# Kernel tuning notes

Measured on AMD Instinct MI355X. Metric: run time of the kernel, lower is better.

## Reference

```python
import jax, jax.numpy as jnp
import numpy as np


def setup_inputs() -> dict:
    key = jax.random.key(0)
    ks = jax.random.split(key, 5)
    B, C, T, Hh, Ww = 4, 64, 8, 32, 32
    HID = 32
    s = 0.05  # weight scale for numerically sane softmax logits
    return {
        "H": jax.random.normal(ks[0], (B, C, T, Hh, Ww), dtype=jnp.float32),
        "h": jax.random.normal(ks[1], (B, C, Hh, Ww), dtype=jnp.float32),
        "w_q": jax.random.normal(ks[2], (HID, C), dtype=jnp.float32) * s,
        "w_kv": jax.random.normal(ks[3], (HID, C), dtype=jnp.float32) * s,
        "w_o": jax.random.normal(ks[4], (C, HID), dtype=jnp.float32) * s,
    }


def reference(H, h, w_q, w_kv, w_o):
    B, C, T, Hh, Ww = H.shape
    N = Hh * Ww
    Hf = H.reshape(B, C, T, N)
    # 1x1 convs are pure channel-mixing matmuls
    H_kv = jnp.einsum('dc,bctn->bdtn', w_kv, Hf)                # [B, hid, T, N]
    h_q = jnp.einsum('dc,bchw->bdhw', w_q, h).reshape(B, -1, N)  # [B, hid, N]
    h_q = h_q.transpose(0, 2, 1)                                 # [B, N, hid]
    # per-timestep scores, vectorized over t: [B, T, N, N]
    a = jnp.einsum('bnd,bdtm->btnm', h_q, H_kv)
    # remove the diagonal of each per-timestep [N, N] block
    diag = jnp.einsum('btnn->btn', a)                            # [B, T, N]
    eye = jnp.eye(N, dtype=a.dtype)
    a = a - diag[..., :, None] * eye
    # concat over t along rows, softmax over the (T*N) row axis
    att = jax.nn.softmax(a.reshape(B, T * N, N), axis=1)         # [B, T*N, N]
    h_v = jnp.einsum('bdk,bkm->bdm', H_kv.reshape(B, -1, T * N), att)  # [B, hid, N]
    h_v = jnp.einsum('cd,bdhw->bchw', w_o, h_v.reshape(B, -1, Hh, Ww))
    return (h + h_v, att)
```

## Files before the change

### kernel.cpp

```cpp
#include <hip/hip_runtime.h>

typedef short bf16x8 __attribute__((ext_vector_type(8)));
typedef float f32x4  __attribute__((ext_vector_type(4)));
typedef unsigned short ushort_t;

#define HID 32
#define CC  64
#define TT  8
#define NN  1024
#define BB  4
#define KTOT 8192

__device__ __forceinline__ ushort_t f2b(float x) {
    unsigned int u = __float_as_uint(x);
    return (ushort_t)((u + 0x7fffu + ((u >> 16) & 1u)) >> 16);
}
__device__ __forceinline__ float b2f(ushort_t u) {
    return __uint_as_float((unsigned int)u << 16);
}

__global__ __launch_bounds__(256) void k_pre(const float* __restrict__ H,
                                             const float* __restrict__ h,
                                             const float* __restrict__ wq,
                                             const float* __restrict__ wkv,
                                             ushort_t* __restrict__ hqHI,
                                             ushort_t* __restrict__ hqLO,
                                             ushort_t* __restrict__ hkTH0,
                                             ushort_t* __restrict__ hkTH1,
                                             ushort_t* __restrict__ hkTL0,
                                             ushort_t* __restrict__ hkTL1,
                                             ushort_t* __restrict__ hkDB) {
    int bx = blockIdx.x;
    if (bx < 256) {
        int gid = bx * 256 + threadIdx.x;
        int dg = gid >> 15;
        int rest = gid & 32767;
        int b = rest >> 13, tn = rest & 8191;
        int d0 = dg << 4;
        float acc[16];
#pragma unroll
        for (int d = 0; d < 16; d++) acc[d] = 0.f;
        const float* Hb = H + (size_t)(b * CC) * KTOT + tn;
        const float* wb = wkv + d0 * CC;
#pragma unroll 8
        for (int c = 0; c < CC; c++) {
            float v = Hb[(size_t)c * KTOT];
#pragma unroll
            for (int d = 0; d < 16; d++) acc[d] += wb[d * CC + c] * v;
        }
        ushort_t thi[16], tlo[16];
#pragma unroll
        for (int d = 0; d < 16; d++) {
            ushort_t hi = f2b(acc[d]);
            thi[d] = hi;
            tlo[d] = f2b(acc[d] - b2f(hi));
        }
        size_t po = ((size_t)b * KTOT + tn) * 16;
        bf16x8* ohi = (bf16x8*)((dg ? hkTH1 : hkTH0) + po);
        bf16x8* olo = (bf16x8*)((dg ? hkTL1 : hkTL0) + po);
#pragma unroll
        for (int v8 = 0; v8 < 2; v8++) {
            bf16x8 a, l;
#pragma unroll
            for (int j = 0; j < 8; j++) { a[j] = (short)thi[v8*8+j]; l[j] = (short)tlo[v8*8+j]; }
            ohi[v8] = a; olo[v8] = l;
        }
#pragma unroll
        for (int d = 0; d < 16; d++)
            hkDB[((size_t)(b * HID) + d0 + d) * KTOT + tn] = thi[d];
    } else {
        int gid = (bx - 256) * 256 + threadIdx.x;
        int b = gid >> 10;
        float acc[HID];
#pragma unroll
        for (int d = 0; d < HID; d++) acc[d] = 0.f;
        const float* hb = h + (size_t)(b * CC) * NN + (gid & 1023);
#pragma unroll 4
        for (int c = 0; c < CC; c++) {
            float v = hb[c * NN];
#pragma unroll
            for (int d = 0; d < HID; d++) acc[d] += wq[d * CC + c] * v;
        }
        bf16x8* ohi = (bf16x8*)(hqHI + (size_t)gid * HID);
        bf16x8* olo = (bf16x8*)(hqLO + (size_t)gid * HID);
#pragma unroll
        for (int v8 = 0; v8 < 4; v8++) {
            bf16x8 thi, tlo;
#pragma unroll
            for (int j = 0; j < 8; j++) {
                float x = acc[v8 * 8 + j];
                ushort_t hi = f2b(x);
                thi[j] = (short)hi;
                tlo[j] = (short)f2b(x - b2f(hi));
            }
            ohi[v8] = thi; olo[v8] = tlo;
        }
    }
}

__global__ __launch_bounds__(1024) void k_fuse(const ushort_t* __restrict__ hqHI,
                                               const ushort_t* __restrict__ hqLO,
                                               const ushort_t* __restrict__ hkTH0,
                                               const ushort_t* __restrict__ hkTH1,
                                               const ushort_t* __restrict__ hkTL0,
                                               const ushort_t* __restrict__ hkTL1,
                                               const ushort_t* __restrict__ hkDB,
                                               float* __restrict__ att,
                                               float* __restrict__ hv2) {
    int bx = blockIdx.x;
    int b = bx >> 6, mt = bx & 63;
    int mb = mt << 4;
    int tid = threadIdx.x;
    int wave = tid >> 6, lane = tid & 63;
    int g = lane >> 4, c = lane & 15;
    int t = wave >> 1;
    int nh = (wave & 1) << 9;

    __shared__ float csred[16][16];
    __shared__ float hvred[16][16][32];
    __shared__ __align__(16) ushort_t PT[16][16][40];

    size_t ako = ((size_t)b * KTOT + t * NN + (mb + c)) * 16 + (g & 1) * 8;
    bf16x8 akh = *(const bf16x8*)(((g >> 1) ? hkTH1 : hkTH0) + ako);
    bf16x8 akl = *(const bf16x8*)(((g >> 1) ? hkTL1 : hkTL0) + ako);

    const ushort_t* qhi = hqHI + ((size_t)(b << 10)) * HID;
    const ushort_t* qlo = hqLO + ((size_t)(b << 10)) * HID;

    f32x4 cs = {0.f, 0.f, 0.f, 0.f};
    for (int s16 = 0; s16 < 32; s16 += 2) {
        int nbA = nh + s16 * 16, nbB = nbA + 16;
        size_t aoA = (size_t)(nbA + c) * HID + 8 * g;
        size_t aoB = (size_t)(nbB + c) * HID + 8 * g;
        bf16x8 qhA = *(const bf16x8*)(qhi + aoA);
        bf16x8 qlA = *(const bf16x8*)(qlo + aoA);
        bf16x8 qhB = *(const bf16x8*)(qhi + aoB);
        bf16x8 qlB = *(const bf16x8*)(qlo + aoB);
        f32x4 svA = __builtin_amdgcn_mfma_f32_16x16x32_bf16(akh, qlA, (f32x4){0.f,0.f,0.f,0.f}, 0, 0, 0);
        f32x4 svB = __builtin_amdgcn_mfma_f32_16x16x32_bf16(akh, qlB, (f32x4){0.f,0.f,0.f,0.f}, 0, 0, 0);
        svA = __builtin_amdgcn_mfma_f32_16x16x32_bf16(akl, qhA, svA, 0, 0, 0);
        svB = __builtin_amdgcn_mfma_f32_16x16x32_bf16(akl, qhB, svB, 0, 0, 0);
        svA = __builtin_amdgcn_mfma_f32_16x16x32_bf16(akh, qhA, svA, 0, 0, 0);
        svB = __builtin_amdgcn_mfma_f32_16x16x32_bf16(akh, qhB, svB, 0, 0, 0);
        int nA = nbA + c, nB = nbB + c;
#pragma unroll
        for (int r = 0; r < 4; r++) {
            float xA = (nA == mb + 4 * g + r) ? 0.f : svA[r];
            float xB = (nB == mb + 4 * g + r) ? 0.f : svB[r];
            cs[r] += __expf(xA) + __expf(xB);
        }
    }
#pragma unroll
    for (int off = 1; off <= 8; off <<= 1) {
#pragma unroll
        for (int r = 0; r < 4; r++) cs[r] += __shfl_xor(cs[r], off, 64);
    }
    if (c == 0) *(f32x4*)&csred[wave][4 * g] = cs;
    __syncthreads();
    f32x4 gs = {0.f, 0.f, 0.f, 0.f};
#pragma unroll
    for (int w = 0; w < 16; w++)
        gs += *(const f32x4*)&csred[w][4 * g];
    f32x4 vinv;
#pragma unroll
    for (int r = 0; r < 4; r++) vinv[r] = 1.0f / gs[r];

    const ushort_t* vb0 = hkDB + (size_t)(b * HID + c) * KTOT;
    const ushort_t* vb1 = hkDB + (size_t)(b * HID + 16 + c) * KTOT;
    float* attb = att + (size_t)b * KTOT * NN;
    ushort_t (*pt)[40] = PT[wave];

    f32x4 acc0 = {0.f,0.f,0.f,0.f}, acc1 = {0.f,0.f,0.f,0.f};

    for (int ks = 0; ks < 16; ks++) {
        int k0 = t * NN + nh + ks * 32;
#pragma unroll
        for (int half = 0; half < 2; half++) {
            int nb = nh + ks * 32 + half * 16;
            size_t qo = (size_t)(nb + c) * HID + 8 * g;
            bf16x8 qh = *(const bf16x8*)(qhi + qo);
            bf16x8 ql = *(const bf16x8*)(qlo + qo);
            f32x4 sv = __builtin_amdgcn_mfma_f32_16x16x32_bf16(akh, ql, (f32x4){0.f,0.f,0.f,0.f}, 0, 0, 0);
            sv = __builtin_amdgcn_mfma_f32_16x16x32_bf16(akl, qh, sv, 0, 0, 0);
            sv = __builtin_amdgcn_mfma_f32_16x16x32_bf16(akh, qh, sv, 0, 0, 0);
            int n = nb + c;
            float e0, e1, e2, e3;
            {
                float x0 = (n == mb + 4 * g + 0) ? 0.f : sv[0];
                float x1 = (n == mb + 4 * g + 1) ? 0.f : sv[1];
                float x2 = (n == mb + 4 * g + 2) ? 0.f : sv[2];
                float x3 = (n == mb + 4 * g + 3) ? 0.f : sv[3];
                e0 = __expf(x0) * vinv[0];
                e1 = __expf(x1) * vinv[1];
                e2 = __expf(x2) * vinv[2];
                e3 = __expf(x3) * vinv[3];
            }
            f32x4 ev; ev[0] = e0; ev[1] = e1; ev[2] = e2; ev[3] = e3;
            __builtin_nontemporal_store(ev,
                (f32x4*)(attb + (size_t)(t * NN + n) * NN + mb + 4 * g));
            int kl = half * 16 + c;
            pt[4 * g + 0][kl] = f2b(e0);
            pt[4 * g + 1][kl] = f2b(e1);
            pt[4 * g + 2][kl] = f2b(e2);
            pt[4 * g + 3][kl] = f2b(e3);
        }
        bf16x8 pa = *(const bf16x8*)&pt[c][8 * g];
        bf16x8 v0 = *(const bf16x8*)(vb0 + k0 + 8 * g);
        bf16x8 v1 = *(const bf16x8*)(vb1 + k0 + 8 * g);
        acc0 = __builtin_amdgcn_mfma_f32_16x16x32_bf16(pa, v0, acc0, 0, 0, 0);
        acc1 = __builtin_amdgcn_mfma_f32_16x16x32_bf16(pa, v1, acc1, 0, 0, 0);
    }

#pragma unroll
    for (int r = 0; r < 4; r++) {
        hvred[wave][4 * g + r][c]      = acc0[r];
        hvred[wave][4 * g + r][16 + c] = acc1[r];
    }
    __syncthreads();
    if (tid < 512) {
        int m = tid >> 5, d = tid & 31;
        float s = 0.f;
#pragma unroll
        for (int w = 0; w < 16; w++) s += hvred[w][m][d];
        hv2[((size_t)(b << 10) + mb + m) * HID + d] = s;
    }
}

__global__ __launch_bounds__(512) void k_out(const float* __restrict__ h,
                                             const float* __restrict__ wo,
                                             const float* __restrict__ hv2,
                                             float* __restrict__ out0) {
    int bx = blockIdx.x;
    int b = bx >> 6, mt = bx & 63;
    int m0 = mt * 16;
    int tid = threadIdx.x;
    __shared__ float hvL[16][33];
    {
        int mm = tid >> 5, d = tid & 31;
        hvL[mm][d] = hv2[((size_t)(b << 10) + m0 + mm) * HID + d];
    }
    __syncthreads();
#pragma unroll
    for (int i0 = 0; i0 < 2; i0++) {
        int i = i0 * 512 + tid;
        int c = i >> 4, mm = i & 15;
        float v = h[(size_t)(b * CC + c) * NN + m0 + mm];
#pragma unroll
        for (int d = 0; d < HID; d++) v += wo[c * HID + d] * hvL[mm][d];
        out0[(size_t)(b * CC + c) * NN + m0 + mm] = v;
    }
}

extern "C" void kernel_launch(void* const* d_in, const int* in_sizes, int n_in,
                              void* d_out, int out_size, void* d_ws, size_t ws_size,
                              hipStream_t stream) {
    const float* H   = (const float*)d_in[0];
    const float* h   = (const float*)d_in[1];
    const float* wq  = (const float*)d_in[2];
    const float* wkv = (const float*)d_in[3];
    const float* wo  = (const float*)d_in[4];

    float* out0 = (float*)d_out;
    float* att  = out0 + (size_t)BB * CC * NN;

    ushort_t* hqHI  = (ushort_t*)d_ws;
    ushort_t* hqLO  = hqHI  + 131072;
    ushort_t* hkTH0 = hqLO  + 131072;
    ushort_t* hkTH1 = hkTH0 + 524288;
    ushort_t* hkTL0 = hkTH1 + 524288;
    ushort_t* hkTL1 = hkTL0 + 524288;
    ushort_t* hkDB  = hkTL1 + 524288;
    float* hv2  = (float*)(hkDB + 1048576);

    k_pre <<<272, 256,  0, stream>>>(H, h, wq, wkv, hqHI, hqLO,
                                     hkTH0, hkTH1, hkTL0, hkTL1, hkDB);
    k_fuse<<<256, 1024, 0, stream>>>(hqHI, hqLO, hkTH0, hkTH1, hkTL0, hkTL1, hkDB,
                                     att, hv2);
    k_out <<<256, 512,  0, stream>>>(h, wo, hv2, out0);
}
```

Before: 88.50 us.

## Fuse softmax denominator pass with PV accumulation and defer normalization

The separate first pass that only computed column sums of exp is removed. Sums now accumulate inside the P·V loop, which uses a single hi-only bf16 MFMA for the scores, and the 1/sum scaling is applied to the accumulator afterwards. A third loop recomputes the full-precision scores to write the normalized attention output. The block index is also remapped to interleave batches across blocks. The hi-only scores make the denominator and hv slightly less accurate than the stored att values, and the att write no longer overlaps the PV MFMA work.

```diff
diff --git a/kernel.cpp b/kernel.cpp
--- a/kernel.cpp
+++ b/kernel.cpp
@@ -108,7 +108,8 @@
                                                float* __restrict__ att,
                                                float* __restrict__ hv2) {
     int bx = blockIdx.x;
-    int b = bx >> 6, mt = bx & 63;
+    int logical = ((bx & 7) << 5) | (bx >> 3);
+    int b = logical >> 6, mt = logical & 63;
     int mb = mt << 4;
     int tid = threadIdx.x;
     int wave = tid >> 6, lane = tid & 63;
@@ -126,52 +127,12 @@
 
     const ushort_t* qhi = hqHI + ((size_t)(b << 10)) * HID;
     const ushort_t* qlo = hqLO + ((size_t)(b << 10)) * HID;
-
-    f32x4 cs = {0.f, 0.f, 0.f, 0.f};
-    for (int s16 = 0; s16 < 32; s16 += 2) {
-        int nbA = nh + s16 * 16, nbB = nbA + 16;
-        size_t aoA = (size_t)(nbA + c) * HID + 8 * g;
-        size_t aoB = (size_t)(nbB + c) * HID + 8 * g;
-        bf16x8 qhA = *(const bf16x8*)(qhi + aoA);
-        bf16x8 qlA = *(const bf16x8*)(qlo + aoA);
-        bf16x8 qhB = *(const bf16x8*)(qhi + aoB);
-        bf16x8 qlB = *(const bf16x8*)(qlo + aoB);
-        f32x4 svA = __builtin_amdgcn_mfma_f32_16x16x32_bf16(akh, qlA, (f32x4){0.f,0.f,0.f,0.f}, 0, 0, 0);
-        f32x4 svB = __builtin_amdgcn_mfma_f32_16x16x32_bf16(akh, qlB, (f32x4){0.f,0.f,0.f,0.f}, 0, 0, 0);
-        svA = __builtin_amdgcn_mfma_f32_16x16x32_bf16(akl, qhA, svA, 0, 0, 0);
-        svB = __builtin_amdgcn_mfma_f32_16x16x32_bf16(akl, qhB, svB, 0, 0, 0);
-        svA = __builtin_amdgcn_mfma_f32_16x16x32_bf16(akh, qhA, svA, 0, 0, 0);
-        svB = __builtin_amdgcn_mfma_f32_16x16x32_bf16(akh, qhB, svB, 0, 0, 0);
-        int nA = nbA + c, nB = nbB + c;
-#pragma unroll
-        for (int r = 0; r < 4; r++) {
-            float xA = (nA == mb + 4 * g + r) ? 0.f : svA[r];
-            float xB = (nB == mb + 4 * g + r) ? 0.f : svB[r];
-            cs[r] += __expf(xA) + __expf(xB);
-        }
-    }
-#pragma unroll
-    for (int off = 1; off <= 8; off <<= 1) {
-#pragma unroll
-        for (int r = 0; r < 4; r++) cs[r] += __shfl_xor(cs[r], off, 64);
-    }
-    if (c == 0) *(f32x4*)&csred[wave][4 * g] = cs;
-    __syncthreads();
-    f32x4 gs = {0.f, 0.f, 0.f, 0.f};
-#pragma unroll
-    for (int w = 0; w < 16; w++)
-        gs += *(const f32x4*)&csred[w][4 * g];
-    f32x4 vinv;
-#pragma unroll
-    for (int r = 0; r < 4; r++) vinv[r] = 1.0f / gs[r];
-
     const ushort_t* vb0 = hkDB + (size_t)(b * HID + c) * KTOT;
     const ushort_t* vb1 = hkDB + (size_t)(b * HID + 16 + c) * KTOT;
-    float* attb = att + (size_t)b * KTOT * NN;
     ushort_t (*pt)[40] = PT[wave];
 
+    f32x4 cs = {0.f, 0.f, 0.f, 0.f};
     f32x4 acc0 = {0.f,0.f,0.f,0.f}, acc1 = {0.f,0.f,0.f,0.f};
-
     for (int ks = 0; ks < 16; ks++) {
         int k0 = t * NN + nh + ks * 32;
 #pragma unroll
@@ -179,25 +140,13 @@
             int nb = nh + ks * 32 + half * 16;
             size_t qo = (size_t)(nb + c) * HID + 8 * g;
             bf16x8 qh = *(const bf16x8*)(qhi + qo);
-            bf16x8 ql = *(const bf16x8*)(qlo + qo);
-            f32x4 sv = __builtin_amdgcn_mfma_f32_16x16x32_bf16(akh, ql, (f32x4){0.f,0.f,0.f,0.f}, 0, 0, 0);
-            sv = __builtin_amdgcn_mfma_f32_16x16x32_bf16(akl, qh, sv, 0, 0, 0);
-            sv = __builtin_amdgcn_mfma_f32_16x16x32_bf16(akh, qh, sv, 0, 0, 0);
+            f32x4 sv = __builtin_amdgcn_mfma_f32_16x16x32_bf16(akh, qh, (f32x4){0.f,0.f,0.f,0.f}, 0, 0, 0);
             int n = nb + c;
-            float e0, e1, e2, e3;
-            {
-                float x0 = (n == mb + 4 * g + 0) ? 0.f : sv[0];
-                float x1 = (n == mb + 4 * g + 1) ? 0.f : sv[1];
-                float x2 = (n == mb + 4 * g + 2) ? 0.f : sv[2];
-                float x3 = (n == mb + 4 * g + 3) ? 0.f : sv[3];
-                e0 = __expf(x0) * vinv[0];
-                e1 = __expf(x1) * vinv[1];
-                e2 = __expf(x2) * vinv[2];
-                e3 = __expf(x3) * vinv[3];
-            }
-            f32x4 ev; ev[0] = e0; ev[1] = e1; ev[2] = e2; ev[3] = e3;
-            __builtin_nontemporal_store(ev,
-                (f32x4*)(attb + (size_t)(t * NN + n) * NN + mb + 4 * g));
+            float e0 = __expf((n == mb + 4 * g + 0) ? 0.f : sv[0]);
+            float e1 = __expf((n == mb + 4 * g + 1) ? 0.f : sv[1]);
+            float e2 = __expf((n == mb + 4 * g + 2) ? 0.f : sv[2]);
+            float e3 = __expf((n == mb + 4 * g + 3) ? 0.f : sv[3]);
+            cs[0] += e0; cs[1] += e1; cs[2] += e2; cs[3] += e3;
             int kl = half * 16 + c;
             pt[4 * g + 0][kl] = f2b(e0);
             pt[4 * g + 1][kl] = f2b(e1);
@@ -210,12 +159,49 @@
         acc0 = __builtin_amdgcn_mfma_f32_16x16x32_bf16(pa, v0, acc0, 0, 0, 0);
         acc1 = __builtin_amdgcn_mfma_f32_16x16x32_bf16(pa, v1, acc1, 0, 0, 0);
     }
+#pragma unroll
+    for (int off = 1; off <= 8; off <<= 1) {
+        cs[0] += __shfl_xor(cs[0], off, 64);
+        cs[1] += __shfl_xor(cs[1], off, 64);
+        cs[2] += __shfl_xor(cs[2], off, 64);
+        cs[3] += __shfl_xor(cs[3], off, 64);
+    }
+    if (c == 0) *(f32x4*)&csred[wave][4 * g] = cs;
+    __syncthreads();
+    f32x4 gs = {0.f, 0.f, 0.f, 0.f};
+#pragma unroll
+    for (int w = 0; w < 16; w++)
+        gs += *(const f32x4*)&csred[w][4 * g];
+    f32x4 vinv;
+#pragma unroll
+    for (int r = 0; r < 4; r++) vinv[r] = 1.0f / gs[r];
 
 #pragma unroll
     for (int r = 0; r < 4; r++) {
-        hvred[wave][4 * g + r][c]      = acc0[r];
-        hvred[wave][4 * g + r][16 + c] = acc1[r];
-    }
+        hvred[wave][4 * g + r][c]      = acc0[r] * vinv[r];
+        hvred[wave][4 * g + r][16 + c] = acc1[r] * vinv[r];
+    }
+
+    float* attb = att + (size_t)b * KTOT * NN;
+#pragma unroll 2
+    for (int hs = 0; hs < 32; hs++) {
+        int nb = nh + hs * 16;
+        size_t qo = (size_t)(nb + c) * HID + 8 * g;
+        bf16x8 qh = *(const bf16x8*)(qhi + qo);
+        bf16x8 ql = *(const bf16x8*)(qlo + qo);
+        f32x4 sv = __builtin_amdgcn_mfma_f32_16x16x32_bf16(akh, ql, (f32x4){0.f,0.f,0.f,0.f}, 0, 0, 0);
+        sv = __builtin_amdgcn_mfma_f32_16x16x32_bf16(akl, qh, sv, 0, 0, 0);
+        sv = __builtin_amdgcn_mfma_f32_16x16x32_bf16(akh, qh, sv, 0, 0, 0);
+        int n = nb + c;
+        f32x4 ev;
+        ev[0] = __expf((n == mb + 4 * g + 0) ? 0.f : sv[0]) * vinv[0];
+        ev[1] = __expf((n == mb + 4 * g + 1) ? 0.f : sv[1]) * vinv[1];
+        ev[2] = __expf((n == mb + 4 * g + 2) ? 0.f : sv[2]) * vinv[2];
+        ev[3] = __expf((n == mb + 4 * g + 3) ? 0.f : sv[3]) * vinv[3];
+        __builtin_nontemporal_store(ev,
+            (f32x4*)(attb + (size_t)(t * NN + n) * NN + mb + 4 * g));
+    }
+
     __syncthreads();
     if (tid < 512) {
         int m = tid >> 5, d = tid & 31;
```

After: 85.06 us. 3.9% less time.
